# Optimization experiments

Hardware: AMD Instinct MI355X
Metric: run time of the kernel (lower is better)

The kernel has to match this reference:

```python
import jax, jax.numpy as jnp
import numpy as np

N_NODES = 100000
N_EDGES = 1600000
N_GRAPHS = 256
HID = 128
NCLS = 3
NEG_SLOPE = 0.2  # DGL GATConv default leaky_relu slope


def gat_layer(h, src, dst, W, al, ar, b):
    # h: [N, Din] -> z: [N, H]
    z = h @ W
    el = z @ al  # [N] attention logits (left / source term)
    er = z @ ar  # [N] attention logits (right / dest term)
    e = jax.nn.leaky_relu(el[src] + er[dst], NEG_SLOPE)  # [E]
    # edge softmax normalized over incoming edges of each dst node
    m = jax.ops.segment_max(e, dst, num_segments=N_NODES)  # [N]
    ex = jnp.exp(e - m[dst])
    s = jax.ops.segment_sum(ex, dst, num_segments=N_NODES)  # [N]
    alpha = ex / jnp.maximum(s[dst], 1e-9)  # [E]
    # scatter-aggregate weighted source features to dst
    out = jax.ops.segment_sum(alpha[:, None] * z[src], dst, num_segments=N_NODES)
    return out + b  # [N, H]


def setup_inputs() -> dict:
    key = jax.random.key(0)
    ks = jax.random.split(key, 16)
    edge_src = jax.random.randint(ks[0], (N_EDGES,), 0, N_NODES)
    edge_dst = jax.random.randint(ks[1], (N_EDGES,), 0, N_NODES)
    graph_ids = jnp.sort(jax.random.randint(ks[2], (N_NODES,), 0, N_GRAPHS))
    sc = 0.1
    return {
        "edge_src": edge_src,
        "edge_dst": edge_dst,
        "graph_ids": graph_ids,
        "W1": jax.random.normal(ks[3], (1, HID), jnp.float32) * sc,
        "al1": jax.random.normal(ks[4], (HID,), jnp.float32) * sc,
        "ar1": jax.random.normal(ks[5], (HID,), jnp.float32) * sc,
        "b1": jax.random.normal(ks[6], (HID,), jnp.float32) * sc,
        "W2": jax.random.normal(ks[7], (HID, HID), jnp.float32) * sc,
        "al2": jax.random.normal(ks[8], (HID,), jnp.float32) * sc,
        "ar2": jax.random.normal(ks[9], (HID,), jnp.float32) * sc,
        "b2": jax.random.normal(ks[10], (HID,), jnp.float32) * sc,
        "Wc": jax.random.normal(ks[11], (HID, NCLS), jnp.float32) * sc,
        "bc": jax.random.normal(ks[12], (NCLS,), jnp.float32) * sc,
    }


def reference(edge_src, edge_dst, graph_ids, W1, al1, ar1, b1, W2, al2, ar2, b2, Wc, bc):
    # initial node features = in-degree, shape [N, 1]
    indeg = jax.ops.segment_sum(jnp.ones((N_EDGES,), jnp.float32), edge_dst,
                                num_segments=N_NODES)
    h = indeg[:, None]
    h = jax.nn.elu(gat_layer(h, edge_src, edge_dst, W1, al1, ar1, b1))
    h = jax.nn.elu(gat_layer(h, edge_src, edge_dst, W2, al2, ar2, b2))
    # dgl.mean_nodes: per-graph mean readout
    sums = jax.ops.segment_sum(h, graph_ids, num_segments=N_GRAPHS)  # [G, H]
    cnts = jax.ops.segment_sum(jnp.ones((N_NODES,), jnp.float32), graph_ids,
                               num_segments=N_GRAPHS)
    hg = sums / jnp.maximum(cnts, 1.0)[:, None]
    return hg @ Wc + bc  # [G, num_classes]
```

## Files before the change

kernel.cpp:

```cpp
#include <hip/hip_runtime.h>
#include <cstdint>
#include <cstddef>

#define N_NODES 100000
#define N_EDGES 1600000
#define N_GRAPHS 256
#define HID 128
#define NCLASS 8
#define MAXD 128

#define SCHUNK 2048
#define SNB ((N_NODES + SCHUNK - 1) / SCHUNK)

static __device__ __forceinline__ float lrelu(float x) { return x >= 0.f ? x : 0.2f * x; }
static __device__ __forceinline__ float elu_f(float x) { return x > 0.f ? x : expm1f(x); }
static __device__ __forceinline__ unsigned f2bf(float x) {
    union { float f; unsigned u; } v; v.f = x;
    return (v.u + 0x7FFFu + ((v.u >> 16) & 1u)) >> 16;
}
static __device__ __forceinline__ float bf_lo(unsigned u) { return __uint_as_float(u << 16); }
static __device__ __forceinline__ float bf_hi(unsigned u) { return __uint_as_float(u & 0xFFFF0000u); }

__global__ void k_prep(const float* __restrict__ W1, const float* __restrict__ al1,
                       const float* __restrict__ ar1, float* __restrict__ scal) {
    int l = threadIdx.x;
    float pl = W1[l] * al1[l] + W1[l + 64] * al1[l + 64];
    float pr = W1[l] * ar1[l] + W1[l + 64] * ar1[l + 64];
    for (int m = 32; m >= 1; m >>= 1) { pl += __shfl_xor(pl, m); pr += __shfl_xor(pr, m); }
    if (l == 0) { scal[0] = pl; scal[1] = pr; }
}

__global__ void k_degrank(const int* __restrict__ dst, int* __restrict__ dr,
                          int* __restrict__ rank) {
    int i = blockIdx.x * blockDim.x + threadIdx.x;
    int st = gridDim.x * blockDim.x;
    for (; i < N_EDGES; i += st) {
        int cls = (i >> 8) & (NCLASS - 1);
        rank[i] = atomicAdd(&dr[cls * N_NODES + dst[i]], 1);
    }
}

__global__ void k_sum(const int* __restrict__ dr, int* __restrict__ deg) {
    int d = blockIdx.x * blockDim.x + threadIdx.x;
    if (d < N_NODES) {
        int s = 0;
#pragma unroll
        for (int r = 0; r < NCLASS; r++) s += dr[r * N_NODES + d];
        deg[d] = s;
    }
}

__global__ void k_scan_part(const int* __restrict__ deg, int* __restrict__ P) {
    __shared__ int sh[256];
    int base = blockIdx.x * SCHUNK + threadIdx.x * 8;
    int s = 0;
#pragma unroll
    for (int e = 0; e < 8; e++) { int idx = base + e; if (idx < N_NODES) s += deg[idx]; }
    sh[threadIdx.x] = s; __syncthreads();
    for (int d = 128; d >= 1; d >>= 1) {
        if (threadIdx.x < d) sh[threadIdx.x] += sh[threadIdx.x + d];
        __syncthreads();
    }
    if (threadIdx.x == 0) P[blockIdx.x] = sh[0];
}

__global__ void k_scan_p2(const int* __restrict__ P, int* __restrict__ P2, int* __restrict__ offs) {
    if (threadIdx.x == 0) {
        int run = 0;
        for (int b = 0; b < SNB; b++) { P2[b] = run; run += P[b]; }
        offs[N_NODES] = run;
    }
}

__global__ void k_scan_final(const int* __restrict__ deg, const int* __restrict__ P2,
                             int* __restrict__ offs) {
    __shared__ int sh[256];
    int base = blockIdx.x * SCHUNK + threadIdx.x * 8;
    int loc[8]; int s = 0;
#pragma unroll
    for (int e = 0; e < 8; e++) {
        int idx = base + e;
        loc[e] = (idx < N_NODES) ? deg[idx] : 0;
        s += loc[e];
    }
    int own = s;
    sh[threadIdx.x] = s; __syncthreads();
    for (int d = 1; d < 256; d <<= 1) {
        int v = (threadIdx.x >= (unsigned)d) ? sh[threadIdx.x - d] : 0;
        __syncthreads();
        sh[threadIdx.x] += v;
        __syncthreads();
    }
    int run = P2[blockIdx.x] + sh[threadIdx.x] - own;
#pragma unroll
    for (int e = 0; e < 8; e++) {
        int idx = base + e;
        if (idx < N_NODES) { offs[idx] = run; run += loc[e]; }
    }
}

__global__ void k_base(const int* __restrict__ dr, const int* __restrict__ offs,
                       int* __restrict__ base) {
    int d = blockIdx.x * blockDim.x + threadIdx.x;
    if (d < N_NODES) {
        int run = offs[d];
#pragma unroll
        for (int r = 0; r < NCLASS; r++) { base[r * N_NODES + d] = run; run += dr[r * N_NODES + d]; }
    }
}

__global__ void k_fill(const int* __restrict__ src, const int* __restrict__ dst,
                       const int* __restrict__ base, const int* __restrict__ rank,
                       int* __restrict__ csr) {
    int i = blockIdx.x * blockDim.x + threadIdx.x;
    int st = gridDim.x * blockDim.x;
    for (; i < N_EDGES; i += st) {
        int cls = (i >> 8) & (NCLASS - 1);
        int pos = base[cls * N_NODES + dst[i]] + rank[i];
        csr[pos] = src[i];
    }
}

__global__ __launch_bounds__(256) void k_l1(const int* __restrict__ deg, const int* __restrict__ offs,
                                            const int* __restrict__ csr_src, const float* __restrict__ scal,
                                            float* __restrict__ t) {
    int node = blockIdx.x * 4 + (threadIdx.x >> 6);
    if (node >= N_NODES) return;
    int l = threadIdx.x & 63;
    float cl = scal[0], cr = scal[1];
    float eri = cr * (float)deg[node];
    int off = offs[node], end = offs[node + 1];
    float m = -INFINITY, den = 0.f, num = 0.f;
    for (int e = off + l; e < end; e += 64) {
        int s = csr_src[e];
        float ds = (float)deg[s];
        float e1 = lrelu(cl * ds + eri);
        if (e1 > m) { float c = __expf(m - e1); den *= c; num *= c; m = e1; }
        float w = __expf(e1 - m);
        den += w; num += w * ds;
    }
    for (int st = 1; st < 64; st <<= 1) {
        float mo = __shfl_xor(m, st);
        float dn = __shfl_xor(den, st);
        float no = __shfl_xor(num, st);
        float mn = fmaxf(m, mo);
        float sa = (m  > -1e37f) ? __expf(m  - mn) : 0.f;
        float sb = (mo > -1e37f) ? __expf(mo - mn) : 0.f;
        den = den * sa + dn * sb;
        num = num * sa + no * sb;
        m = mn;
    }
    if (l == 0) t[node] = num / fmaxf(den, 1e-9f);
}

__global__ __launch_bounds__(256, 4) void k_gemm(
    const float* __restrict__ t, const float* __restrict__ W1, const float* __restrict__ b1,
    const float* __restrict__ W2, const float* __restrict__ al2, const float* __restrict__ ar2,
    unsigned* __restrict__ zb, float* __restrict__ el2, float* __restrict__ er2) {
    __shared__ float h1s[8][8][HID];
    __shared__ float W1s[HID], b1s[HID], al2s[HID], ar2s[HID];
    if (threadIdx.x < HID) {
        W1s[threadIdx.x] = W1[threadIdx.x]; b1s[threadIdx.x] = b1[threadIdx.x];
        al2s[threadIdx.x] = al2[threadIdx.x]; ar2s[threadIdx.x] = ar2[threadIdx.x];
    }
    __syncthreads();
    int g = threadIdx.x >> 5;
    int lt = threadIdx.x & 31;
    const float4* W2v = (const float4*)W2;
    for (int i0 = blockIdx.x * 64; i0 < N_NODES; i0 += gridDim.x * 64) {
        int ibase = i0 + g * 8;
        for (int n = 0; n < 8; n++) {
            int i = ibase + n;
            if (i < N_NODES) {
                float ti = t[i];
                float4 hv;
                hv.x = elu_f(ti * W1s[4 * lt + 0] + b1s[4 * lt + 0]);
                hv.y = elu_f(ti * W1s[4 * lt + 1] + b1s[4 * lt + 1]);
                hv.z = elu_f(ti * W1s[4 * lt + 2] + b1s[4 * lt + 2]);
                hv.w = elu_f(ti * W1s[4 * lt + 3] + b1s[4 * lt + 3]);
                *(float4*)&h1s[g][n][4 * lt] = hv;
            }
        }
        __syncthreads();
        float4 acc[8];
#pragma unroll
        for (int n = 0; n < 8; n++) acc[n] = make_float4(0.f, 0.f, 0.f, 0.f);
        for (int j = 0; j < HID / 4; j++) {
            float4 w0 = W2v[(4 * j + 0) * 32 + lt];
            float4 w1 = W2v[(4 * j + 1) * 32 + lt];
            float4 w2 = W2v[(4 * j + 2) * 32 + lt];
            float4 w3 = W2v[(4 * j + 3) * 32 + lt];
#pragma unroll
            for (int n = 0; n < 8; n++) {
                float4 hv = *(const float4*)&h1s[g][n][4 * j];
                acc[n].x += hv.x * w0.x + hv.y * w1.x + hv.z * w2.x + hv.w * w3.x;
                acc[n].y += hv.x * w0.y + hv.y * w1.y + hv.z * w2.y + hv.w * w3.y;
                acc[n].z += hv.x * w0.z + hv.y * w1.z + hv.z * w2.z + hv.w * w3.z;
                acc[n].w += hv.x * w0.w + hv.y * w1.w + hv.z * w2.w + hv.w * w3.w;
            }
        }
#pragma unroll
        for (int n = 0; n < 8; n++) {
            int i = ibase + n;
            if (i < N_NODES) {
                float4 a = acc[n];
                uint2 st;
                st.x = f2bf(a.x) | (f2bf(a.y) << 16);
                st.y = f2bf(a.z) | (f2bf(a.w) << 16);
                *(uint2*)&zb[(size_t)i * 64 + 2 * lt] = st;
                float pl = a.x * al2s[4 * lt] + a.y * al2s[4 * lt + 1] +
                           a.z * al2s[4 * lt + 2] + a.w * al2s[4 * lt + 3];
                float pr = a.x * ar2s[4 * lt] + a.y * ar2s[4 * lt + 1] +
                           a.z * ar2s[4 * lt + 2] + a.w * ar2s[4 * lt + 3];
                for (int mm = 16; mm >= 1; mm >>= 1) { pl += __shfl_xor(pl, mm); pr += __shfl_xor(pr, mm); }
                if (lt == 0) { el2[i] = pl; er2[i] = pr; }
            }
        }
        __syncthreads();
    }
}

__global__ __launch_bounds__(256) void k_l2f(
    const int* __restrict__ offs, const int* __restrict__ csr_src,
    const float* __restrict__ el2, const float* __restrict__ er2,
    const unsigned* __restrict__ zb, const float* __restrict__ b2,
    float* __restrict__ h2) {
    __shared__ float wbuf[4][MAXD];
    __shared__ int   sbuf[4][MAXD];
    int wv = threadIdx.x >> 6;
    int node = blockIdx.x * 4 + wv;
    if (node >= N_NODES) return;
    int l = threadIdx.x & 63;
    float eri = er2[node];
    int off = offs[node], end = offs[node + 1];
    int deg = end - off;
    int ndeg = min(deg, MAXD);
    float mx = -INFINITY;
    for (int j = l; j < deg; j += 64) {
        int s = csr_src[off + j];
        float x = el2[s] + eri;
        float e2 = lrelu(x);
        if (j < MAXD) { sbuf[wv][j] = s; wbuf[wv][j] = e2; }
        mx = fmaxf(mx, e2);
    }
    for (int st = 1; st < 64; st <<= 1) mx = fmaxf(mx, __shfl_xor(mx, st));
    float den = 0.f;
    for (int j = l; j < ndeg; j += 64) {
        float w = __expf(wbuf[wv][j] - mx);
        wbuf[wv][j] = w;
        den += w;
    }
    for (int j = MAXD + l; j < deg; j += 64) {
        int s = csr_src[off + j];
        den += __expf(lrelu(el2[s] + eri) - mx);
    }
    for (int st = 1; st < 64; st <<= 1) den += __shfl_xor(den, st);
    float rden = 1.f / fmaxf(den, 1e-9f);
    float a0 = 0.f, a1 = 0.f;
    int j = 0;
    for (; j + 4 <= ndeg; j += 4) {
        float4 w4 = *(const float4*)&wbuf[wv][j];
        int4   s4 = *(const int4*)&sbuf[wv][j];
        unsigned z0 = zb[((unsigned)s4.x << 6) + l];
        unsigned z1 = zb[((unsigned)s4.y << 6) + l];
        unsigned z2 = zb[((unsigned)s4.z << 6) + l];
        unsigned z3 = zb[((unsigned)s4.w << 6) + l];
        a0 += w4.x * bf_lo(z0) + w4.y * bf_lo(z1) + w4.z * bf_lo(z2) + w4.w * bf_lo(z3);
        a1 += w4.x * bf_hi(z0) + w4.y * bf_hi(z1) + w4.z * bf_hi(z2) + w4.w * bf_hi(z3);
    }
    for (; j < ndeg; j++) {
        float w = wbuf[wv][j];
        unsigned z = zb[((unsigned)sbuf[wv][j] << 6) + l];
        a0 += w * bf_lo(z);
        a1 += w * bf_hi(z);
    }
    for (int j2 = MAXD; j2 < deg; j2++) {
        int s = csr_src[off + j2];
        float w = __expf(lrelu(el2[s] + eri) - mx);
        unsigned z = zb[((unsigned)s << 6) + l];
        a0 += w * bf_lo(z);
        a1 += w * bf_hi(z);
    }
    float2 bb = *(const float2*)&b2[2 * l];
    float2 o;
    o.x = elu_f(a0 * rden + bb.x);
    o.y = elu_f(a1 * rden + bb.y);
    *(float2*)&h2[(size_t)node * HID + 2 * l] = o;
}

static __device__ __forceinline__ int lower_bound_i(const int* a, int n, int v) {
    int lo = 0, hi = n;
    while (lo < hi) { int mid = (lo + hi) >> 1; if (a[mid] < v) lo = mid + 1; else hi = mid; }
    return lo;
}

__global__ __launch_bounds__(1024) void k_pool(const int* __restrict__ gids, const float* __restrict__ h2,
                                               const float* __restrict__ Wc, const float* __restrict__ bc,
                                               float* __restrict__ out) {
    int g = blockIdx.x;
    int lo = lower_bound_i(gids, N_NODES, g);
    int hi = lower_bound_i(gids, N_NODES, g + 1);
    int j = threadIdx.x & 127;
    int nn = threadIdx.x >> 7;
    float s = 0.f;
    for (int n = lo + nn; n < hi; n += 8) s += h2[(size_t)n * HID + j];
    __shared__ float red[1024];
    red[threadIdx.x] = s;
    __syncthreads();
    __shared__ float red2[2][3];
    if (threadIdx.x < 128) {
        float hg = 0.f;
#pragma unroll
        for (int q = 0; q < 8; q++) hg += red[q * 128 + j];
        hg /= fmaxf((float)(hi - lo), 1.f);
        float p0 = hg * Wc[j * 3 + 0];
        float p1 = hg * Wc[j * 3 + 1];
        float p2 = hg * Wc[j * 3 + 2];
        for (int mm = 32; mm >= 1; mm >>= 1) {
            p0 += __shfl_xor(p0, mm); p1 += __shfl_xor(p1, mm); p2 += __shfl_xor(p2, mm);
        }
        if ((threadIdx.x & 63) == 0) {
            int w = threadIdx.x >> 6;
            red2[w][0] = p0; red2[w][1] = p1; red2[w][2] = p2;
        }
    }
    __syncthreads();
    if (threadIdx.x < 3)
        out[g * 3 + threadIdx.x] = red2[0][threadIdx.x] + red2[1][threadIdx.x] + bc[threadIdx.x];
}

extern "C" void kernel_launch(void* const* d_in, const int* in_sizes, int n_in,
                              void* d_out, int out_size, void* d_ws, size_t ws_size,
                              hipStream_t stream) {
    (void)in_sizes; (void)n_in; (void)out_size; (void)ws_size;
    const int* edge_src = (const int*)d_in[0];
    const int* edge_dst = (const int*)d_in[1];
    const int* gids     = (const int*)d_in[2];
    const float* W1  = (const float*)d_in[3];
    const float* al1 = (const float*)d_in[4];
    const float* ar1 = (const float*)d_in[5];
    const float* b1  = (const float*)d_in[6];
    const float* W2  = (const float*)d_in[7];
    const float* al2 = (const float*)d_in[8];
    const float* ar2 = (const float*)d_in[9];
    const float* b2  = (const float*)d_in[10];
    const float* Wc  = (const float*)d_in[11];
    const float* bc  = (const float*)d_in[12];
    float* out = (float*)d_out;

    char* p = (char*)d_ws;
    auto alloc = [&](size_t bytes) -> char* {
        char* r = p;
        p += (bytes + 511) & ~(size_t)511;
        return r;
    };
    int*      dr    = (int*)alloc((size_t)NCLASS * N_NODES * 4);
    int*      base  = (int*)alloc((size_t)NCLASS * N_NODES * 4);
    int*      rank  = (int*)alloc((size_t)N_EDGES * 4);
    int*      offs  = (int*)alloc((size_t)(N_NODES + 1) * 4);
    int*      P     = (int*)alloc((size_t)SNB * 4);
    int*      P2    = (int*)alloc((size_t)SNB * 4);
    float*    scal  = (float*)alloc(64);
    int*      csr   = (int*)alloc((size_t)N_EDGES * 4);
    int*      deg   = (int*)alloc((size_t)N_NODES * 4);
    float*    t     = (float*)alloc((size_t)N_NODES * 4);
    float*    el2   = (float*)alloc((size_t)N_NODES * 4);
    float*    er2   = (float*)alloc((size_t)N_NODES * 4);
    unsigned* zb    = (unsigned*)alloc((size_t)N_NODES * 64 * 4);
    float*    h2    = (float*)alloc((size_t)N_NODES * HID * 4);

    hipMemsetAsync(dr, 0, (size_t)NCLASS * N_NODES * 4, stream);

    k_prep<<<1, 64, 0, stream>>>(W1, al1, ar1, scal);
    k_degrank<<<2048, 256, 0, stream>>>(edge_dst, dr, rank);
    k_sum<<<(N_NODES + 255) / 256, 256, 0, stream>>>(dr, deg);
    k_scan_part<<<SNB, 256, 0, stream>>>(deg, P);
    k_scan_p2<<<1, 64, 0, stream>>>(P, P2, offs);
    k_scan_final<<<SNB, 256, 0, stream>>>(deg, P2, offs);
    k_base<<<(N_NODES + 255) / 256, 256, 0, stream>>>(dr, offs, base);
    k_fill<<<2048, 256, 0, stream>>>(edge_src, edge_dst, base, rank, csr);
    k_l1<<<(N_NODES + 3) / 4, 256, 0, stream>>>(deg, offs, csr, scal, t);
    k_gemm<<<(N_NODES + 63) / 64, 256, 0, stream>>>(t, W1, b1, W2, al2, ar2, zb, el2, er2);
    k_l2f<<<(N_NODES + 3) / 4, 256, 0, stream>>>(offs, csr, el2, er2, zb, b2, h2);
    k_pool<<<N_GRAPHS, 1024, 0, stream>>>(gids, h2, Wc, bc, out);
}
```

Measured before the change: 382.6 us.

## Use bf16 MFMA for layer-2 GEMM with swizzled transposed W2 in LDS

Replaces the scalar FP32 FMA GEMM in k_gemm with bf16 MFMA 16x16x32 instructions. W2 is converted to bf16, transposed and XOR-swizzled into shared memory once per block, and each lane builds its A fragment directly from the ELU of the layer-1 output. The grid becomes a fixed persistent size that loops over node tiles, and the per-tile LDS staging and barriers are removed. The el2/er2 dot products and the bf16 z stores are recomputed from the MFMA accumulator layout. The bf16 inputs lower the precision of the matmul, and each block now pays a one-time W2 load and transpose.

```diff
diff --git a/kernel.cpp b/kernel.cpp
--- a/kernel.cpp
+++ b/kernel.cpp
@@ -8,9 +8,13 @@
 #define HID 128
 #define NCLASS 8
 #define MAXD 128
+#define GEMM_GRID 782
 
 #define SCHUNK 2048
 #define SNB ((N_NODES + SCHUNK - 1) / SCHUNK)
+
+typedef short bf16x8 __attribute__((ext_vector_type(8)));
+typedef float f32x4 __attribute__((ext_vector_type(4)));
 
 static __device__ __forceinline__ float lrelu(float x) { return x >= 0.f ? x : 0.2f * x; }
 static __device__ __forceinline__ float elu_f(float x) { return x > 0.f ? x : expm1f(x); }
@@ -153,70 +157,106 @@
     if (l == 0) t[node] = num / fmaxf(den, 1e-9f);
 }
 
-__global__ __launch_bounds__(256, 4) void k_gemm(
+__global__ __launch_bounds__(256, 3) void k_gemm(
     const float* __restrict__ t, const float* __restrict__ W1, const float* __restrict__ b1,
     const float* __restrict__ W2, const float* __restrict__ al2, const float* __restrict__ ar2,
     unsigned* __restrict__ zb, float* __restrict__ el2, float* __restrict__ er2) {
-    __shared__ float h1s[8][8][HID];
+    __shared__ unsigned short W2t[HID * HID];
     __shared__ float W1s[HID], b1s[HID], al2s[HID], ar2s[HID];
-    if (threadIdx.x < HID) {
-        W1s[threadIdx.x] = W1[threadIdx.x]; b1s[threadIdx.x] = b1[threadIdx.x];
-        al2s[threadIdx.x] = al2[threadIdx.x]; ar2s[threadIdx.x] = ar2[threadIdx.x];
+    int tid = threadIdx.x;
+    if (tid < HID) {
+        W1s[tid] = W1[tid]; b1s[tid] = b1[tid];
+        al2s[tid] = al2[tid]; ar2s[tid] = ar2[tid];
+    }
+    const float4* W2v = (const float4*)W2;
+    for (int q = tid; q < HID * HID / 4; q += 256) {
+        int k = q >> 5;
+        int c0 = (q & 31) << 2;
+        float4 w = W2v[q];
+        W2t[((c0 + 0) * HID + k) ^ (((c0 + 0) & 7) << 3)] = (unsigned short)f2bf(w.x);
+        W2t[((c0 + 1) * HID + k) ^ (((c0 + 1) & 7) << 3)] = (unsigned short)f2bf(w.y);
+        W2t[((c0 + 2) * HID + k) ^ (((c0 + 2) & 7) << 3)] = (unsigned short)f2bf(w.z);
+        W2t[((c0 + 3) * HID + k) ^ (((c0 + 3) & 7) << 3)] = (unsigned short)f2bf(w.w);
     }
     __syncthreads();
-    int g = threadIdx.x >> 5;
-    int lt = threadIdx.x & 31;
-    const float4* W2v = (const float4*)W2;
+    int wid = tid >> 6, lane = tid & 63;
+    int nl = lane & 15;
+    int kq = lane >> 4;
     for (int i0 = blockIdx.x * 64; i0 < N_NODES; i0 += gridDim.x * 64) {
-        int ibase = i0 + g * 8;
-        for (int n = 0; n < 8; n++) {
-            int i = ibase + n;
-            if (i < N_NODES) {
-                float ti = t[i];
-                float4 hv;
-                hv.x = elu_f(ti * W1s[4 * lt + 0] + b1s[4 * lt + 0]);
-                hv.y = elu_f(ti * W1s[4 * lt + 1] + b1s[4 * lt + 1]);
-                hv.z = elu_f(ti * W1s[4 * lt + 2] + b1s[4 * lt + 2]);
-                hv.w = elu_f(ti * W1s[4 * lt + 3] + b1s[4 * lt + 3]);
-                *(float4*)&h1s[g][n][4 * lt] = hv;
+        int node = i0 + wid * 16 + nl;
+        float tval = (node < N_NODES) ? t[node] : 0.f;
+        f32x4 acc[8];
+#pragma unroll
+        for (int c = 0; c < 8; c++) acc[c] = (f32x4){0.f, 0.f, 0.f, 0.f};
+#pragma unroll
+        for (int s = 0; s < 4; s++) {
+            int kb = s * 32 + kq * 8;
+            float4 wa = *(const float4*)&W1s[kb];
+            float4 wb = *(const float4*)&W1s[kb + 4];
+            float4 ba = *(const float4*)&b1s[kb];
+            float4 bb = *(const float4*)&b1s[kb + 4];
+            float h0 = elu_f(tval * wa.x + ba.x);
+            float h1 = elu_f(tval * wa.y + ba.y);
+            float h2 = elu_f(tval * wa.z + ba.z);
+            float h3 = elu_f(tval * wa.w + ba.w);
+            float h4 = elu_f(tval * wb.x + bb.x);
+            float h5 = elu_f(tval * wb.y + bb.y);
+            float h6 = elu_f(tval * wb.z + bb.z);
+            float h7 = elu_f(tval * wb.w + bb.w);
+            union { unsigned u[4]; bf16x8 v; } afr;
+            afr.u[0] = f2bf(h0) | (f2bf(h1) << 16);
+            afr.u[1] = f2bf(h2) | (f2bf(h3) << 16);
+            afr.u[2] = f2bf(h4) | (f2bf(h5) << 16);
+            afr.u[3] = f2bf(h6) | (f2bf(h7) << 16);
+#pragma unroll
+            for (int c = 0; c < 8; c++) {
+                int col = c * 16 + nl;
+                int idx = (col * HID + kb) ^ ((col & 7) << 3);
+                bf16x8 bfr = *(const bf16x8*)&W2t[idx];
+                acc[c] = __builtin_amdgcn_mfma_f32_16x16x32_bf16(afr.v, bfr, acc[c], 0, 0, 0);
             }
         }
-        __syncthreads();
-        float4 acc[8];
-#pragma unroll
-        for (int n = 0; n < 8; n++) acc[n] = make_float4(0.f, 0.f, 0.f, 0.f);
-        for (int j = 0; j < HID / 4; j++) {
-            float4 w0 = W2v[(4 * j + 0) * 32 + lt];
-            float4 w1 = W2v[(4 * j + 1) * 32 + lt];
-            float4 w2 = W2v[(4 * j + 2) * 32 + lt];
-            float4 w3 = W2v[(4 * j + 3) * 32 + lt];
-#pragma unroll
-            for (int n = 0; n < 8; n++) {
-                float4 hv = *(const float4*)&h1s[g][n][4 * j];
-                acc[n].x += hv.x * w0.x + hv.y * w1.x + hv.z * w2.x + hv.w * w3.x;
-                acc[n].y += hv.x * w0.y + hv.y * w1.y + hv.z * w2.y + hv.w * w3.y;
-                acc[n].z += hv.x * w0.z + hv.y * w1.z + hv.z * w2.z + hv.w * w3.z;
-                acc[n].w += hv.x * w0.w + hv.y * w1.w + hv.z * w2.w + hv.w * w3.w;
+        int rnode = i0 + wid * 16 + kq * 4;
+        float plv[4] = {0.f, 0.f, 0.f, 0.f}, prv[4] = {0.f, 0.f, 0.f, 0.f};
+#pragma unroll
+        for (int c = 0; c < 8; c++) {
+            float av = al2s[c * 16 + nl], rv = ar2s[c * 16 + nl];
+#pragma unroll
+            for (int r = 0; r < 4; r++) {
+                plv[r] += acc[c][r] * av;
+                prv[r] += acc[c][r] * rv;
             }
         }
 #pragma unroll
-        for (int n = 0; n < 8; n++) {
-            int i = ibase + n;
-            if (i < N_NODES) {
-                float4 a = acc[n];
-                uint2 st;
-                st.x = f2bf(a.x) | (f2bf(a.y) << 16);
-                st.y = f2bf(a.z) | (f2bf(a.w) << 16);
-                *(uint2*)&zb[(size_t)i * 64 + 2 * lt] = st;
-                float pl = a.x * al2s[4 * lt] + a.y * al2s[4 * lt + 1] +
-                           a.z * al2s[4 * lt + 2] + a.w * al2s[4 * lt + 3];
-                float pr = a.x * ar2s[4 * lt] + a.y * ar2s[4 * lt + 1] +
-                           a.z * ar2s[4 * lt + 2] + a.w * ar2s[4 * lt + 3];
-                for (int mm = 16; mm >= 1; mm >>= 1) { pl += __shfl_xor(pl, mm); pr += __shfl_xor(pr, mm); }
-                if (lt == 0) { el2[i] = pl; er2[i] = pr; }
+        for (int r = 0; r < 4; r++) {
+#pragma unroll
+            for (int m = 1; m < 16; m <<= 1) {
+                plv[r] += __shfl_xor(plv[r], m);
+                prv[r] += __shfl_xor(prv[r], m);
             }
         }
-        __syncthreads();
+        if (nl == 0) {
+#pragma unroll
+            for (int r = 0; r < 4; r++) {
+                int n2 = rnode + r;
+                if (n2 < N_NODES) { el2[n2] = plv[r]; er2[n2] = prv[r]; }
+            }
+        }
+#pragma unroll
+        for (int c = 0; c < 8; c++) {
+#pragma unroll
+            for (int r = 0; r < 4; r++) {
+                float v = acc[c][r];
+                float v2 = __shfl_xor(v, 1);
+                if (!(lane & 1)) {
+                    int n2 = rnode + r;
+                    if (n2 < N_NODES) {
+                        unsigned u = f2bf(v) | (f2bf(v2) << 16);
+                        zb[(size_t)n2 * 64 + c * 8 + (nl >> 1)] = u;
+                    }
+                }
+            }
+        }
     }
 }
 
@@ -380,7 +420,7 @@
     k_base<<<(N_NODES + 255) / 256, 256, 0, stream>>>(dr, offs, base);
     k_fill<<<2048, 256, 0, stream>>>(edge_src, edge_dst, base, rank, csr);
     k_l1<<<(N_NODES + 3) / 4, 256, 0, stream>>>(deg, offs, csr, scal, t);
-    k_gemm<<<(N_NODES + 63) / 64, 256, 0, stream>>>(t, W1, b1, W2, al2, ar2, zb, el2, er2);
+    k_gemm<<<GEMM_GRID, 256, 0, stream>>>(t, W1, b1, W2, al2, ar2, zb, el2, er2);
     k_l2f<<<(N_NODES + 3) / 4, 256, 0, stream>>>(offs, csr, el2, er2, zb, b2, h2);
     k_pool<<<N_GRAPHS, 1024, 0, stream>>>(gids, h2, Wc, bc, out);
 }
```

After: 382.9 us. About the same (+0.1%).
